# Kernel optimization log

Hardware: AMD Instinct MI355X
Metric: run time of the kernel (lower is better)

The kernel has to match this reference:

```python
import jax, jax.numpy as jnp
import numpy as np

GRID_SIZE = 5
SPLINE_ORDER = 3
HIDDEN = 128
N = 131072
K = 256          # num_cluster
EPS = 1e-8       # torch.cosine_similarity eps
N_COEF = GRID_SIZE + SPLINE_ORDER  # 8 spline basis functions per input feature


def make_grid():
    # efficient-kan grid: grid_range [-1,1], extended by spline_order on each side
    h = 2.0 / GRID_SIZE
    g = jnp.arange(-SPLINE_ORDER, GRID_SIZE + SPLINE_ORDER + 1, dtype=jnp.float32) * h - 1.0
    return jnp.tile(g[None, :], (HIDDEN, 1))  # (in, grid_size + 2*order + 1) = (128, 12)


def b_splines(x, grid):
    # x: (N, in), grid: (in, G) -> bases: (N, in, grid_size + spline_order)
    xe = x[..., None]
    bases = ((xe >= grid[:, :-1]) & (xe < grid[:, 1:])).astype(x.dtype)
    for p in range(1, SPLINE_ORDER + 1):
        left = (xe - grid[:, :-(p + 1)]) / (grid[:, p:-1] - grid[:, :-(p + 1)])
        right = (grid[:, p + 1:] - xe) / (grid[:, p + 1:] - grid[:, 1:-p])
        bases = left * bases[..., :-1] + right * bases[..., 1:]
    return bases


def kan_linear(x, grid, base_w, spline_w, scaler):
    # efficient-kan KANLinear: base path + spline path
    base = jax.nn.silu(x) @ base_w.T                       # (N, out)
    sp = b_splines(x, grid)                                # (N, in, coef)
    sw = spline_w * scaler[..., None]                      # (out, in, coef)
    return base + jnp.einsum('nic,oic->no', sp, sw)


def setup_inputs() -> dict:
    key = jax.random.key(0)
    ks = jax.random.split(key, 9)
    s = 1.0 / np.sqrt(HIDDEN)
    return {
        'x': jax.random.normal(ks[0], (N, HIDDEN), jnp.float32),
        'prototypes': jax.random.normal(ks[1], (K, HIDDEN), jnp.float32),
        'grid': make_grid(),
        'base_w1': jax.random.normal(ks[2], (HIDDEN, HIDDEN), jnp.float32) * s,
        'spline_w1': jax.random.normal(ks[3], (HIDDEN, HIDDEN, N_COEF), jnp.float32) * 0.1,
        'scaler1': jax.random.normal(ks[4], (HIDDEN, HIDDEN), jnp.float32) * s + 1.0,
        'base_w2': jax.random.normal(ks[5], (HIDDEN, HIDDEN), jnp.float32) * s,
        'spline_w2': jax.random.normal(ks[6], (HIDDEN, HIDDEN, N_COEF), jnp.float32) * 0.1,
        'scaler2': jax.random.normal(ks[7], (HIDDEN, HIDDEN), jnp.float32) * s + 1.0,
    }


def reference(x, prototypes, grid, base_w1, spline_w1, scaler1, base_w2, spline_w2, scaler2):
    # KAN([128,128,128]) = two KANLinear layers
    h = kan_linear(x, grid, base_w1, spline_w1, scaler1)
    emb = kan_linear(h, grid, base_w2, spline_w2, scaler2)     # (N, 128)
    # cosine similarity to all prototypes = normalized matmul (same math as
    # the broadcasted torch.cosine_similarity, without the (N,K,H) intermediate)
    xn = emb / jnp.maximum(jnp.linalg.norm(emb, axis=-1, keepdims=True), EPS)
    pn = prototypes / jnp.maximum(jnp.linalg.norm(prototypes, axis=-1, keepdims=True), EPS)
    sim = xn @ pn.T                                            # (N, K)
    cluster_assignments = jnp.argmax(sim, axis=1)              # (N,)
    return emb, cluster_assignments
```

## Files before the change

kernel.cpp:

```cpp
#include <hip/hip_runtime.h>
#include <math.h>

typedef unsigned short u16;
typedef _Float16 f16;
typedef __attribute__((ext_vector_type(8))) _Float16 f16x8;
typedef __attribute__((ext_vector_type(2))) _Float16 f16x2;
typedef __attribute__((ext_vector_type(4))) float f32x4;

#define N_ROWS 131072
#define HID 128
#define WS_CH 8192
#define N_WCH 72
#define N_PCH 8

__device__ __forceinline__ void split8(const float* a8, f16x8& hv, f16x8& lv) {
    union { f16x8 v; f16x2 p[4]; } H, L;
    #pragma unroll
    for (int j = 0; j < 4; ++j) {
        float v0 = a8[2 * j], v1 = a8[2 * j + 1];
        float h0 = __builtin_bit_cast(float, __builtin_bit_cast(unsigned, v0) & 0xFFFFE000u);
        float h1 = __builtin_bit_cast(float, __builtin_bit_cast(unsigned, v1) & 0xFFFFE000u);
        H.p[j] = __builtin_bit_cast(f16x2, __builtin_amdgcn_cvt_pkrtz(v0, v1));
        L.p[j] = __builtin_bit_cast(f16x2, __builtin_amdgcn_cvt_pkrtz(v0 - h0, v1 - h1));
    }
    hv = H.v; lv = L.v;
}

__device__ __forceinline__ void spline8(float xv, float* a8) {
    float s  = (xv + 2.2f) * 2.5f;
    float tf = floorf(s);
    int   tt = (int)tf;
    bool valid = (tt >= 0) && (tt <= 10);
    float kt = (float)(tt - 3) * 0.4f - 1.0f;
    float u  = (xv - kt) * 2.5f;
    float u2 = u * u, u3 = u2 * u;
    float om = 1.0f - u;
    float b3 = u3 * (1.0f / 6.0f);
    float b2 = (-3.f * u3 + 3.f * u2 + 3.f * u + 1.f) * (1.0f / 6.0f);
    float b1 = (3.f * u3 - 6.f * u2 + 4.f) * (1.0f / 6.0f);
    float b0 = om * om * om * (1.0f / 6.0f);
    #pragma unroll
    for (int c = 0; c < 8; ++c) {
        int d = tt - c;
        float v = 0.f;
        v = (d == 0) ? b3 : v;
        v = (d == 1) ? b2 : v;
        v = (d == 2) ? b1 : v;
        v = (d == 3) ? b0 : v;
        a8[c] = valid ? v : 0.f;
    }
}

__device__ __forceinline__ int tswz(int r, int c) {
    return (r << 7) + ((((c >> 2) ^ r) & 31) << 2) + (c & 3);
}

__global__ __launch_bounds__(256)
void pack_weights(const float* __restrict__ bw1, const float* __restrict__ sw1,
                  const float* __restrict__ sc1,
                  const float* __restrict__ bw2, const float* __restrict__ sw2,
                  const float* __restrict__ sc2,
                  const float* __restrict__ protos, u16* __restrict__ ws)
{
    int gid = blockIdx.x * 256 + threadIdx.x;
    if (gid < N_WCH * 4096) {
        int l  = gid / (36 * 4096);
        int r  = gid % (36 * 4096);
        int ch = r / 4096;
        int e  = r % 4096;
        int o  = e >> 5;
        int kl = e & 31;
        const float* bw = l ? bw2 : bw1;
        const float* sw = l ? sw2 : sw1;
        const float* sc = l ? sc2 : sc1;
        float v;
        if (ch < 4) {
            v = bw[o * HID + ch * 32 + kl];
        } else {
            int i = (ch - 4) * 4 + (kl >> 3);
            v = sw[(o * HID + i) * 8 + (kl & 7)] * sc[o * HID + i];
        }
        f16 hi = (f16)v;
        f16 lo = (f16)(v - (float)hi);
        int nt = o >> 4, n = o & 15, kq = kl >> 3, c = kl & 7;
        size_t base = (size_t)(l * 36 + ch) * WS_CH;
        size_t idx  = ((size_t)nt * 64 + kq * 16 + n) * 8 + c;
        ws[base + idx]        = __builtin_bit_cast(u16, hi);
        ws[base + 4096 + idx] = __builtin_bit_cast(u16, lo);
    } else if (gid < (N_WCH + N_PCH) * 4096) {
        int r  = gid - N_WCH * 4096;
        int hk = r / 4096;
        int e  = r % 4096;
        int pl = e >> 5;
        int kl = e & 31;
        int half = hk >> 2, kc = hk & 3;
        int p = half * 128 + pl;
        const float4 pv = *(const float4*)(protos + (size_t)p * HID + kl * 4);
        float s = pv.x * pv.x + pv.y * pv.y + pv.z * pv.z + pv.w * pv.w;
        #pragma unroll
        for (int off = 1; off < 32; off <<= 1) s += __shfl_xor(s, off);
        float rp = 1.0f / fmaxf(sqrtf(s), 1e-8f);
        float v = protos[(size_t)p * HID + kc * 32 + kl] * rp;
        f16 hi = (f16)v;
        f16 lo = (f16)(v - (float)hi);
        int nt = pl >> 4, n = pl & 15, kq = kl >> 3, c = kl & 7;
        size_t base = (size_t)(N_WCH + hk) * WS_CH;
        size_t idx  = ((size_t)nt * 64 + kq * 16 + n) * 8 + c;
        ws[base + idx]        = __builtin_bit_cast(u16, hi);
        ws[base + 4096 + idx] = __builtin_bit_cast(u16, lo);
    }
}

__global__ __launch_bounds__(256, 2)
void kan_fused(const float* __restrict__ x, const u16* __restrict__ wpack,
               float* __restrict__ emb_out, float* __restrict__ assign_out)
{
    __shared__ float t[128 * 128];
    __shared__ u16   Bfrag[2][8][64][8];

    const int tid  = threadIdx.x;
    const int lane = tid & 63;
    const int w    = tid >> 6;
    const int m    = lane & 15;
    const int q    = lane >> 4;
    const int row0 = w * 32 + m;
    const int brow = blockIdx.x * 128;

    const char* gptr = (const char*)wpack + (size_t)w * 4096 + (size_t)lane * 16;
    uint4* const lptr = (uint4*)&Bfrag[0][0][0][0] + w * 256 + lane;
    uint4 rr0, rr1, rr2, rr3;

#define ISSUE_LOADS() do {                                                         \
        rr0 = *(const uint4*)(gptr);                                               \
        rr1 = *(const uint4*)(gptr + 1024);                                        \
        rr2 = *(const uint4*)(gptr + 2048);                                        \
        rr3 = *(const uint4*)(gptr + 3072);                                        \
        gptr += 16384;                                                             \
    } while (0)

#define STORE_LDS() do {                                                           \
        lptr[0] = rr0; lptr[64] = rr1; lptr[128] = rr2; lptr[192] = rr3;           \
    } while (0)

#define PIPE_BARRIER() do {                                                        \
        asm volatile("s_waitcnt lgkmcnt(0)" ::: "memory");                         \
        __builtin_amdgcn_s_barrier();                                              \
        __builtin_amdgcn_sched_barrier(0);                                         \
    } while (0)

    ISSUE_LOADS();

    {
        const int m2 = tid >> 1, hf = tid & 1;
        const float4* src = (const float4*)(x + (size_t)(brow + m2) * HID + hf * 64);
        #pragma unroll
        for (int j = 0; j < 16; ++j) {
            float4 v = src[j];
            *(float4*)&t[tswz(m2, hf * 64 + j * 4)] = v;
        }
    }

    f16x8 ah0, al0, ah1, al1, bhv, blv;
    f32x4 acc0[8], acc1[8];

    for (int l = 0; l < 2; ++l) {
        #pragma unroll
        for (int nt = 0; nt < 8; ++nt) {
            acc0[nt] = (f32x4){0.f, 0.f, 0.f, 0.f};
            acc1[nt] = (f32x4){0.f, 0.f, 0.f, 0.f};
        }

        for (int ch = 0; ch < 36; ++ch) {
            float a80[8], a81[8];
            if (ch < 4) {
                float4 u0 = *(const float4*)&t[tswz(row0, ch * 32 + q * 8)];
                float4 u1 = *(const float4*)&t[tswz(row0, ch * 32 + q * 8 + 4)];
                float4 v0 = *(const float4*)&t[tswz(row0 + 16, ch * 32 + q * 8)];
                float4 v1 = *(const float4*)&t[tswz(row0 + 16, ch * 32 + q * 8 + 4)];
                float xs0[8] = {u0.x, u0.y, u0.z, u0.w, u1.x, u1.y, u1.z, u1.w};
                float xs1[8] = {v0.x, v0.y, v0.z, v0.w, v1.x, v1.y, v1.z, v1.w};
                #pragma unroll
                for (int j = 0; j < 8; ++j) {
                    a80[j] = xs0[j] * __builtin_amdgcn_rcpf(1.0f + __expf(-xs0[j]));
                    a81[j] = xs1[j] * __builtin_amdgcn_rcpf(1.0f + __expf(-xs1[j]));
                }
            } else {
                spline8(t[tswz(row0,      (ch - 4) * 4 + q)], a80);
                spline8(t[tswz(row0 + 16, (ch - 4) * 4 + q)], a81);
            }
            split8(a80, ah0, al0);
            split8(a81, ah1, al1);

            PIPE_BARRIER();
            STORE_LDS();
            ISSUE_LOADS();
            PIPE_BARRIER();

            __builtin_amdgcn_s_setprio(1);
            #pragma unroll
            for (int nt = 0; nt < 8; ++nt) {
                bhv = *(const f16x8*)Bfrag[0][nt][lane];
                blv = *(const f16x8*)Bfrag[1][nt][lane];
                acc0[nt] = __builtin_amdgcn_mfma_f32_16x16x32_f16(ah0, bhv, acc0[nt], 0, 0, 0);
                acc0[nt] = __builtin_amdgcn_mfma_f32_16x16x32_f16(al0, bhv, acc0[nt], 0, 0, 0);
                acc0[nt] = __builtin_amdgcn_mfma_f32_16x16x32_f16(ah0, blv, acc0[nt], 0, 0, 0);
                acc1[nt] = __builtin_amdgcn_mfma_f32_16x16x32_f16(ah1, bhv, acc1[nt], 0, 0, 0);
                acc1[nt] = __builtin_amdgcn_mfma_f32_16x16x32_f16(al1, bhv, acc1[nt], 0, 0, 0);
                acc1[nt] = __builtin_amdgcn_mfma_f32_16x16x32_f16(ah1, blv, acc1[nt], 0, 0, 0);
            }
            __builtin_amdgcn_s_setprio(0);
        }

        #pragma unroll
        for (int nt = 0; nt < 8; ++nt)
            #pragma unroll
            for (int r = 0; r < 4; ++r) {
                t[tswz(w * 32 + q * 4 + r,      nt * 16 + m)] = acc0[nt][r];
                t[tswz(w * 32 + 16 + q * 4 + r, nt * 16 + m)] = acc1[nt][r];
            }
    }

    {
        const int m2 = tid >> 1, hf = tid & 1;
        float* dst = emb_out + (size_t)(brow + m2) * HID + hf * 64;
        #pragma unroll
        for (int j = 0; j < 16; ++j)
            *(float4*)(dst + j * 4) = *(const float4*)&t[tswz(m2, hf * 64 + j * 4)];
    }

    float best0[4], best1[4]; int bi0[4], bi1[4];
    #pragma unroll
    for (int r = 0; r < 4; ++r) {
        best0[r] = -3.402823466e+38f; bi0[r] = 0;
        best1[r] = -3.402823466e+38f; bi1[r] = 0;
    }

    for (int half = 0; half < 2; ++half) {
        #pragma unroll
        for (int nt = 0; nt < 8; ++nt) {
            acc0[nt] = (f32x4){0.f, 0.f, 0.f, 0.f};
            acc1[nt] = (f32x4){0.f, 0.f, 0.f, 0.f};
        }

        for (int kc = 0; kc < 4; ++kc) {
            const int reg = N_WCH + half * 4 + kc;

            float a80[8], a81[8];
            {
                float4 u0 = *(const float4*)&t[tswz(row0, kc * 32 + q * 8)];
                float4 u1 = *(const float4*)&t[tswz(row0, kc * 32 + q * 8 + 4)];
                float4 v0 = *(const float4*)&t[tswz(row0 + 16, kc * 32 + q * 8)];
                float4 v1 = *(const float4*)&t[tswz(row0 + 16, kc * 32 + q * 8 + 4)];
                a80[0] = u0.x; a80[1] = u0.y; a80[2] = u0.z; a80[3] = u0.w;
                a80[4] = u1.x; a80[5] = u1.y; a80[6] = u1.z; a80[7] = u1.w;
                a81[0] = v0.x; a81[1] = v0.y; a81[2] = v0.z; a81[3] = v0.w;
                a81[4] = v1.x; a81[5] = v1.y; a81[6] = v1.z; a81[7] = v1.w;
            }
            split8(a80, ah0, al0);
            split8(a81, ah1, al1);

            PIPE_BARRIER();
            STORE_LDS();
            if (reg != 79) ISSUE_LOADS();
            PIPE_BARRIER();

            __builtin_amdgcn_s_setprio(1);
            #pragma unroll
            for (int nt = 0; nt < 8; ++nt) {
                bhv = *(const f16x8*)Bfrag[0][nt][lane];
                blv = *(const f16x8*)Bfrag[1][nt][lane];
                acc0[nt] = __builtin_amdgcn_mfma_f32_16x16x32_f16(ah0, bhv, acc0[nt], 0, 0, 0);
                acc0[nt] = __builtin_amdgcn_mfma_f32_16x16x32_f16(al0, bhv, acc0[nt], 0, 0, 0);
                acc0[nt] = __builtin_amdgcn_mfma_f32_16x16x32_f16(ah0, blv, acc0[nt], 0, 0, 0);
                acc1[nt] = __builtin_amdgcn_mfma_f32_16x16x32_f16(ah1, bhv, acc1[nt], 0, 0, 0);
                acc1[nt] = __builtin_amdgcn_mfma_f32_16x16x32_f16(al1, bhv, acc1[nt], 0, 0, 0);
                acc1[nt] = __builtin_amdgcn_mfma_f32_16x16x32_f16(ah1, blv, acc1[nt], 0, 0, 0);
            }
            __builtin_amdgcn_s_setprio(0);
        }

        #pragma unroll
        for (int nt = 0; nt < 8; ++nt) {
            int p = half * 128 + nt * 16 + m;
            #pragma unroll
            for (int r = 0; r < 4; ++r) {
                float v0 = acc0[nt][r];
                if (v0 > best0[r]) { best0[r] = v0; bi0[r] = p; }
                float v1 = acc1[nt][r];
                if (v1 > best1[r]) { best1[r] = v1; bi1[r] = p; }
            }
        }
    }

    #pragma unroll
    for (int r = 0; r < 4; ++r) {
        #pragma unroll
        for (int off = 1; off < 16; off <<= 1) {
            float ov0 = __shfl_xor(best0[r], off);
            int   oi0 = __shfl_xor(bi0[r], off);
            if (ov0 > best0[r] || (ov0 == best0[r] && oi0 < bi0[r])) { best0[r] = ov0; bi0[r] = oi0; }
            float ov1 = __shfl_xor(best1[r], off);
            int   oi1 = __shfl_xor(bi1[r], off);
            if (ov1 > best1[r] || (ov1 == best1[r] && oi1 < bi1[r])) { best1[r] = ov1; bi1[r] = oi1; }
        }
        if (m == 0) {
            assign_out[(size_t)brow + w * 32 + q * 4 + r]      = (float)bi0[r];
            assign_out[(size_t)brow + w * 32 + 16 + q * 4 + r] = (float)bi1[r];
        }
    }
#undef ISSUE_LOADS
#undef STORE_LDS
#undef PIPE_BARRIER
}

extern "C" void kernel_launch(void* const* d_in, const int* in_sizes, int n_in,
                              void* d_out, int out_size, void* d_ws, size_t ws_size,
                              hipStream_t stream) {
    (void)in_sizes; (void)n_in; (void)out_size; (void)ws_size;

    const float* x      = (const float*)d_in[0];
    const float* protos = (const float*)d_in[1];
    const float* bw1 = (const float*)d_in[3];
    const float* sw1 = (const float*)d_in[4];
    const float* sc1 = (const float*)d_in[5];
    const float* bw2 = (const float*)d_in[6];
    const float* sw2 = (const float*)d_in[7];
    const float* sc2 = (const float*)d_in[8];

    float* out    = (float*)d_out;
    float* embp   = out;
    float* assign = out + (size_t)N_ROWS * HID;
    u16*   wpack  = (u16*)d_ws;

    pack_weights<<<dim3((N_WCH + N_PCH) * 4096 / 256), dim3(256), 0, stream>>>(
        bw1, sw1, sc1, bw2, sw2, sc2, protos, wpack);
    kan_fused<<<dim3(N_ROWS / 128), dim3(256), 0, stream>>>(
        x, wpack, embp, assign);
}
```

Measured before the change: 388.9 us.

## Software-pipeline A-operand prep with MFMA using double-buffered register sets

Restructures the chunk loops so the spline/silu/split preparation for the next K-chunk is computed while the MFMAs for the current chunk are issued, using two alternating register sets (SA/SB). This aims to hide VALU transcendental and spline work behind matrix-core execution instead of serializing them before each barrier. It raises register pressure, which may reduce occupancy or cause spills, and the prep now runs at raised priority.

```diff
diff --git a/kernel.cpp b/kernel.cpp
--- a/kernel.cpp
+++ b/kernel.cpp
@@ -24,6 +24,10 @@
         L.p[j] = __builtin_bit_cast(f16x2, __builtin_amdgcn_cvt_pkrtz(v0 - h0, v1 - h1));
     }
     hv = H.v; lv = L.v;
+}
+
+__device__ __forceinline__ float silu1(float v) {
+    return v * __builtin_amdgcn_rcpf(1.0f + __expf(-v));
 }
 
 __device__ __forceinline__ void spline8(float xv, float* a8) {
@@ -160,56 +164,89 @@
         }
     }
 
-    f16x8 ah0, al0, ah1, al1, bhv, blv;
+    struct ASet { f16x8 h0, l0, h1, l1; };
+    ASet SA, SB;
     f32x4 acc0[8], acc1[8];
 
-    for (int l = 0; l < 2; ++l) {
+    auto bsync = [&](bool issue) {
+        PIPE_BARRIER();
+        STORE_LDS();
+        if (issue) ISSUE_LOADS();
+        PIPE_BARRIER();
+    };
+
+    auto zero_accs = [&]() {
         #pragma unroll
         for (int nt = 0; nt < 8; ++nt) {
             acc0[nt] = (f32x4){0.f, 0.f, 0.f, 0.f};
             acc1[nt] = (f32x4){0.f, 0.f, 0.f, 0.f};
         }
-
-        for (int ch = 0; ch < 36; ++ch) {
-            float a80[8], a81[8];
-            if (ch < 4) {
-                float4 u0 = *(const float4*)&t[tswz(row0, ch * 32 + q * 8)];
-                float4 u1 = *(const float4*)&t[tswz(row0, ch * 32 + q * 8 + 4)];
-                float4 v0 = *(const float4*)&t[tswz(row0 + 16, ch * 32 + q * 8)];
-                float4 v1 = *(const float4*)&t[tswz(row0 + 16, ch * 32 + q * 8 + 4)];
-                float xs0[8] = {u0.x, u0.y, u0.z, u0.w, u1.x, u1.y, u1.z, u1.w};
-                float xs1[8] = {v0.x, v0.y, v0.z, v0.w, v1.x, v1.y, v1.z, v1.w};
-                #pragma unroll
-                for (int j = 0; j < 8; ++j) {
-                    a80[j] = xs0[j] * __builtin_amdgcn_rcpf(1.0f + __expf(-xs0[j]));
-                    a81[j] = xs1[j] * __builtin_amdgcn_rcpf(1.0f + __expf(-xs1[j]));
-                }
-            } else {
-                spline8(t[tswz(row0,      (ch - 4) * 4 + q)], a80);
-                spline8(t[tswz(row0 + 16, (ch - 4) * 4 + q)], a81);
-            }
-            split8(a80, ah0, al0);
-            split8(a81, ah1, al1);
-
-            PIPE_BARRIER();
-            STORE_LDS();
-            ISSUE_LOADS();
-            PIPE_BARRIER();
-
-            __builtin_amdgcn_s_setprio(1);
-            #pragma unroll
-            for (int nt = 0; nt < 8; ++nt) {
-                bhv = *(const f16x8*)Bfrag[0][nt][lane];
-                blv = *(const f16x8*)Bfrag[1][nt][lane];
-                acc0[nt] = __builtin_amdgcn_mfma_f32_16x16x32_f16(ah0, bhv, acc0[nt], 0, 0, 0);
-                acc0[nt] = __builtin_amdgcn_mfma_f32_16x16x32_f16(al0, bhv, acc0[nt], 0, 0, 0);
-                acc0[nt] = __builtin_amdgcn_mfma_f32_16x16x32_f16(ah0, blv, acc0[nt], 0, 0, 0);
-                acc1[nt] = __builtin_amdgcn_mfma_f32_16x16x32_f16(ah1, bhv, acc1[nt], 0, 0, 0);
-                acc1[nt] = __builtin_amdgcn_mfma_f32_16x16x32_f16(al1, bhv, acc1[nt], 0, 0, 0);
-                acc1[nt] = __builtin_amdgcn_mfma_f32_16x16x32_f16(ah1, blv, acc1[nt], 0, 0, 0);
-            }
-            __builtin_amdgcn_s_setprio(0);
-        }
+    };
+
+    auto mfma48 = [&](const ASet& A) {
+        #pragma unroll
+        for (int nt = 0; nt < 8; ++nt) {
+            f16x8 bhv = *(const f16x8*)Bfrag[0][nt][lane];
+            f16x8 blv = *(const f16x8*)Bfrag[1][nt][lane];
+            acc0[nt] = __builtin_amdgcn_mfma_f32_16x16x32_f16(A.h0, bhv, acc0[nt], 0, 0, 0);
+            acc0[nt] = __builtin_amdgcn_mfma_f32_16x16x32_f16(A.l0, bhv, acc0[nt], 0, 0, 0);
+            acc0[nt] = __builtin_amdgcn_mfma_f32_16x16x32_f16(A.h0, blv, acc0[nt], 0, 0, 0);
+            acc1[nt] = __builtin_amdgcn_mfma_f32_16x16x32_f16(A.h1, bhv, acc1[nt], 0, 0, 0);
+            acc1[nt] = __builtin_amdgcn_mfma_f32_16x16x32_f16(A.l1, bhv, acc1[nt], 0, 0, 0);
+            acc1[nt] = __builtin_amdgcn_mfma_f32_16x16x32_f16(A.h1, blv, acc1[nt], 0, 0, 0);
+        }
+    };
+
+    auto prep_silu = [&](int ch, ASet& N) {
+        float a8[8];
+        float4 u0 = *(const float4*)&t[tswz(row0, ch * 32 + q * 8)];
+        float4 u1 = *(const float4*)&t[tswz(row0, ch * 32 + q * 8 + 4)];
+        a8[0] = silu1(u0.x); a8[1] = silu1(u0.y); a8[2] = silu1(u0.z); a8[3] = silu1(u0.w);
+        a8[4] = silu1(u1.x); a8[5] = silu1(u1.y); a8[6] = silu1(u1.z); a8[7] = silu1(u1.w);
+        split8(a8, N.h0, N.l0);
+        float4 v0 = *(const float4*)&t[tswz(row0 + 16, ch * 32 + q * 8)];
+        float4 v1 = *(const float4*)&t[tswz(row0 + 16, ch * 32 + q * 8 + 4)];
+        a8[0] = silu1(v0.x); a8[1] = silu1(v0.y); a8[2] = silu1(v0.z); a8[3] = silu1(v0.w);
+        a8[4] = silu1(v1.x); a8[5] = silu1(v1.y); a8[6] = silu1(v1.z); a8[7] = silu1(v1.w);
+        split8(a8, N.h1, N.l1);
+    };
+    auto prep_spline = [&](int ch, ASet& N) {
+        float s0 = t[tswz(row0,      (ch - 4) * 4 + q)];
+        float s1 = t[tswz(row0 + 16, (ch - 4) * 4 + q)];
+        float a8[8];
+        spline8(s0, a8); split8(a8, N.h0, N.l0);
+        spline8(s1, a8); split8(a8, N.h1, N.l1);
+    };
+    auto prep_pass = [&](int kc, ASet& N) {
+        float a8[8];
+        float4 u0 = *(const float4*)&t[tswz(row0, kc * 32 + q * 8)];
+        float4 u1 = *(const float4*)&t[tswz(row0, kc * 32 + q * 8 + 4)];
+        a8[0] = u0.x; a8[1] = u0.y; a8[2] = u0.z; a8[3] = u0.w;
+        a8[4] = u1.x; a8[5] = u1.y; a8[6] = u1.z; a8[7] = u1.w;
+        split8(a8, N.h0, N.l0);
+        float4 v0 = *(const float4*)&t[tswz(row0 + 16, kc * 32 + q * 8)];
+        float4 v1 = *(const float4*)&t[tswz(row0 + 16, kc * 32 + q * 8 + 4)];
+        a8[0] = v0.x; a8[1] = v0.y; a8[2] = v0.z; a8[3] = v0.w;
+        a8[4] = v1.x; a8[5] = v1.y; a8[6] = v1.z; a8[7] = v1.w;
+        split8(a8, N.h1, N.l1);
+    };
+
+    #define PRIO_ON()  __builtin_amdgcn_s_setprio(1)
+    #define PRIO_OFF() __builtin_amdgcn_s_setprio(0)
+
+    for (int l = 0; l < 2; ++l) {
+        zero_accs();
+        prep_silu(0, SA);
+        bsync(true); PRIO_ON(); mfma48(SA); prep_silu(1, SB); PRIO_OFF();
+        bsync(true); PRIO_ON(); mfma48(SB); prep_silu(2, SA); PRIO_OFF();
+        bsync(true); PRIO_ON(); mfma48(SA); prep_silu(3, SB); PRIO_OFF();
+        bsync(true); PRIO_ON(); mfma48(SB); prep_spline(4, SA); PRIO_OFF();
+        for (int ch = 4; ch < 34; ch += 2) {
+            bsync(true); PRIO_ON(); mfma48(SA); prep_spline(ch + 1, SB); PRIO_OFF();
+            bsync(true); PRIO_ON(); mfma48(SB); prep_spline(ch + 2, SA); PRIO_OFF();
+        }
+        bsync(true); PRIO_ON(); mfma48(SA); prep_spline(35, SB); PRIO_OFF();
+        bsync(true); PRIO_ON(); mfma48(SB); PRIO_OFF();
 
         #pragma unroll
         for (int nt = 0; nt < 8; ++nt)
@@ -235,50 +272,7 @@
         best1[r] = -3.402823466e+38f; bi1[r] = 0;
     }
 
-    for (int half = 0; half < 2; ++half) {
-        #pragma unroll
-        for (int nt = 0; nt < 8; ++nt) {
-            acc0[nt] = (f32x4){0.f, 0.f, 0.f, 0.f};
-            acc1[nt] = (f32x4){0.f, 0.f, 0.f, 0.f};
-        }
-
-        for (int kc = 0; kc < 4; ++kc) {
-            const int reg = N_WCH + half * 4 + kc;
-
-            float a80[8], a81[8];
-            {
-                float4 u0 = *(const float4*)&t[tswz(row0, kc * 32 + q * 8)];
-                float4 u1 = *(const float4*)&t[tswz(row0, kc * 32 + q * 8 + 4)];
-                float4 v0 = *(const float4*)&t[tswz(row0 + 16, kc * 32 + q * 8)];
-                float4 v1 = *(const float4*)&t[tswz(row0 + 16, kc * 32 + q * 8 + 4)];
-                a80[0] = u0.x; a80[1] = u0.y; a80[2] = u0.z; a80[3] = u0.w;
-                a80[4] = u1.x; a80[5] = u1.y; a80[6] = u1.z; a80[7] = u1.w;
-                a81[0] = v0.x; a81[1] = v0.y; a81[2] = v0.z; a81[3] = v0.w;
-                a81[4] = v1.x; a81[5] = v1.y; a81[6] = v1.z; a81[7] = v1.w;
-            }
-            split8(a80, ah0, al0);
-            split8(a81, ah1, al1);
-
-            PIPE_BARRIER();
-            STORE_LDS();
-            if (reg != 79) ISSUE_LOADS();
-            PIPE_BARRIER();
-
-            __builtin_amdgcn_s_setprio(1);
-            #pragma unroll
-            for (int nt = 0; nt < 8; ++nt) {
-                bhv = *(const f16x8*)Bfrag[0][nt][lane];
-                blv = *(const f16x8*)Bfrag[1][nt][lane];
-                acc0[nt] = __builtin_amdgcn_mfma_f32_16x16x32_f16(ah0, bhv, acc0[nt], 0, 0, 0);
-                acc0[nt] = __builtin_amdgcn_mfma_f32_16x16x32_f16(al0, bhv, acc0[nt], 0, 0, 0);
-                acc0[nt] = __builtin_amdgcn_mfma_f32_16x16x32_f16(ah0, blv, acc0[nt], 0, 0, 0);
-                acc1[nt] = __builtin_amdgcn_mfma_f32_16x16x32_f16(ah1, bhv, acc1[nt], 0, 0, 0);
-                acc1[nt] = __builtin_amdgcn_mfma_f32_16x16x32_f16(al1, bhv, acc1[nt], 0, 0, 0);
-                acc1[nt] = __builtin_amdgcn_mfma_f32_16x16x32_f16(ah1, blv, acc1[nt], 0, 0, 0);
-            }
-            __builtin_amdgcn_s_setprio(0);
-        }
-
+    auto reduce_half = [&](int half) {
         #pragma unroll
         for (int nt = 0; nt < 8; ++nt) {
             int p = half * 128 + nt * 16 + m;
@@ -289,8 +283,23 @@
                 float v1 = acc1[nt][r];
                 if (v1 > best1[r]) { best1[r] = v1; bi1[r] = p; }
             }
-        }
-    }
+            acc0[nt] = (f32x4){0.f, 0.f, 0.f, 0.f};
+            acc1[nt] = (f32x4){0.f, 0.f, 0.f, 0.f};
+        }
+    };
+
+    zero_accs();
+    prep_pass(0, SA);
+    bsync(true);  PRIO_ON(); mfma48(SA); prep_pass(1, SB); PRIO_OFF();
+    bsync(true);  PRIO_ON(); mfma48(SB); prep_pass(2, SA); PRIO_OFF();
+    bsync(true);  PRIO_ON(); mfma48(SA); prep_pass(3, SB); PRIO_OFF();
+    bsync(true);  PRIO_ON(); mfma48(SB); prep_pass(0, SA); PRIO_OFF();
+    reduce_half(0);
+    bsync(true);  PRIO_ON(); mfma48(SA); prep_pass(1, SB); PRIO_OFF();
+    bsync(true);  PRIO_ON(); mfma48(SB); prep_pass(2, SA); PRIO_OFF();
+    bsync(true);  PRIO_ON(); mfma48(SA); prep_pass(3, SB); PRIO_OFF();
+    bsync(false); PRIO_ON(); mfma48(SB); PRIO_OFF();
+    reduce_half(1);
 
     #pragma unroll
     for (int r = 0; r < 4; ++r) {
```

New measurement: 390.7 us. Within noise of the previous version (+0.5%).
